# Optimization experiments

Hardware: AMD Instinct MI355X
Metric: run time of the kernel (lower is better)

Reference implementation:

```python
import jax, jax.numpy as jnp
import numpy as np

DIM, DEPTH, MULT = 512, 3, 4
E = 2 ** DEPTH            # 8 experts
HID = MULT * DIM          # 2048
B, S = 4, 1024


def setup_inputs() -> dict:
    key = jax.random.key(0)
    ks = jax.random.split(key, 7)
    sd = 1.0 / np.sqrt(DIM)
    sh = 1.0 / np.sqrt(HID)
    return {
        "x": jax.random.normal(ks[0], (B, S, DIM), dtype=jnp.float32),
        "rw": jax.random.normal(ks[1], (E - 1, DIM), dtype=jnp.float32) * sd,
        "rb": jax.random.normal(ks[2], (E - 1,), dtype=jnp.float32) * sd,
        "w1": jax.random.normal(ks[3], (E, DIM, HID), dtype=jnp.float32) * sd,
        "b1": jax.random.normal(ks[4], (E, HID), dtype=jnp.float32) * sd,
        "w2": jax.random.normal(ks[5], (E, HID, DIM), dtype=jnp.float32) * sh,
        "b2": jax.random.normal(ks[6], (E, DIM), dtype=jnp.float32) * sh,
    }


def _leaf_probs(flat_x, rw, rb):
    # Binary-tree soft routing: level d has 2**d routers at offset 2**d - 1.
    n_tok = flat_x.shape[0]
    leaf = jnp.ones((n_tok, 1), dtype=flat_x.dtype)
    for d in range(DEPTH):
        off, n = 2 ** d - 1, 2 ** d
        logits = flat_x @ rw[off:off + n].T + rb[off:off + n]   # [N, n]
        p = jax.nn.sigmoid(logits)
        # child probs: left = 1-p, right = p
        leaf = (leaf[:, :, None] * jnp.stack([1.0 - p, p], axis=2)).reshape(n_tok, 2 * n)
    return leaf  # [N, E]


def reference(x, rw, rb, w1, b1, w2, b2):
    b, s, dim = x.shape
    flat_x = x.reshape(b * s, dim)                               # [N, D]
    leaf_probs = _leaf_probs(flat_x, rw, rb)                     # [N, E]
    # Dense evaluation of all experts (soft-routing training path).
    h = jnp.einsum('nd,edh->neh', flat_x, w1) + b1[None]         # [N, E, H]
    h = jax.nn.gelu(h, approximate=False)                        # torch nn.GELU (erf)
    y = jnp.einsum('neh,ehd->ned', h, w2) + b2[None]             # [N, E, D]
    out = jnp.einsum('ned,ne->nd', y, leaf_probs)                # [N, D]
    return out.reshape(b, s, dim)
```

## Files before the change

### kernel.cpp

```cpp
#include <hip/hip_runtime.h>
#include <hip/hip_bf16.h>
#include <hip/hip_fp16.h>

#define DIM 512
#define HID 2048
#define NE 8
#define NTOK 4096

typedef _Float16 v8h __attribute__((ext_vector_type(8)));
typedef float v4f __attribute__((ext_vector_type(4)));

__device__ __forceinline__ void load16(const void* g, void* l) {
  __builtin_amdgcn_global_load_lds(
      (const __attribute__((address_space(1))) unsigned int*)g,
      (__attribute__((address_space(3))) unsigned int*)l, 16, 0, 0);
}

__device__ __forceinline__ float gelu_fast(float v) {
  float v2 = v * v;
  float u = v * __builtin_fmaf(0.07135481627f, v2, 1.5957691216f);
  float t = __expf(-u);
  return v * __builtin_amdgcn_rcpf(1.0f + t);
}

__global__ __launch_bounds__(256) void routing_kernel(const float* __restrict__ x,
                                                      const float* __restrict__ rw,
                                                      const float* __restrict__ rb,
                                                      const float* __restrict__ b2,
                                                      float* __restrict__ leaf,
                                                      _Float16* __restrict__ xh,
                                                      float* __restrict__ out) {
  const int lane = threadIdx.x & 63;
  const int wave = threadIdx.x >> 6;
  const int n = (blockIdx.x << 2) + wave;
  const float4* xv = (const float4*)(x + (size_t)n * DIM);
  const float4 x0 = xv[lane * 2], x1 = xv[lane * 2 + 1];
  v8h o;
  o[0] = (_Float16)x0.x; o[1] = (_Float16)x0.y; o[2] = (_Float16)x0.z; o[3] = (_Float16)x0.w;
  o[4] = (_Float16)x1.x; o[5] = (_Float16)x1.y; o[6] = (_Float16)x1.z; o[7] = (_Float16)x1.w;
  *(v8h*)(xh + (size_t)n * DIM + lane * 8) = o;
  float logits[7];
#pragma unroll
  for (int rr = 0; rr < 7; ++rr) {
    const float4* wv = (const float4*)(rw + rr * DIM);
    const float4 w0 = wv[lane * 2], w1v = wv[lane * 2 + 1];
    float s = x0.x * w0.x + x0.y * w0.y + x0.z * w0.z + x0.w * w0.w +
              x1.x * w1v.x + x1.y * w1v.y + x1.z * w1v.z + x1.w * w1v.w;
#pragma unroll
    for (int o2 = 32; o2; o2 >>= 1) s += __shfl_xor(s, o2, 64);
    logits[rr] = s + rb[rr];
  }
  const int eidx = lane & 7;
  const float p0 = 1.f / (1.f + __expf(-logits[0]));
  float f = ((eidx >> 2) & 1) ? p0 : 1.f - p0;
  const float p1 = 1.f / (1.f + __expf(-logits[1 + (eidx >> 2)]));
  f *= ((eidx >> 1) & 1) ? p1 : 1.f - p1;
  const float p2 = 1.f / (1.f + __expf(-logits[3 + (eidx >> 1)]));
  f *= (eidx & 1) ? p2 : 1.f - p2;
  if (lane < NE) leaf[(size_t)n * NE + lane] = f;
  float le[NE];
#pragma unroll
  for (int e = 0; e < NE; ++e) le[e] = __shfl(f, e, 64);
  float4 a0 = {0.f, 0.f, 0.f, 0.f}, a1 = {0.f, 0.f, 0.f, 0.f};
#pragma unroll
  for (int e = 0; e < NE; ++e) {
    const float4* bv = (const float4*)(b2 + (size_t)e * DIM + lane * 8);
    const float4 u0 = bv[0], u1 = bv[1];
    a0.x += le[e] * u0.x; a0.y += le[e] * u0.y; a0.z += le[e] * u0.z; a0.w += le[e] * u0.w;
    a1.x += le[e] * u1.x; a1.y += le[e] * u1.y; a1.z += le[e] * u1.z; a1.w += le[e] * u1.w;
  }
  float4* op = (float4*)(out + (size_t)n * DIM + lane * 8);
  op[0] = a0; op[1] = a1;
}

__global__ __launch_bounds__(256) void transpose_cvt2_kernel(const float* __restrict__ w1,
                                                             _Float16* __restrict__ w1t,
                                                             const float* __restrict__ w2,
                                                             _Float16* __restrict__ w2t) {
  int bx = blockIdx.x;
  const float* in;
  _Float16* outp;
  int R, C;
  if (bx < 4096) { in = w1; outp = w1t; R = DIM; C = HID; }
  else { bx -= 4096; in = w2; outp = w2t; R = HID; C = DIM; }
  const int e = bx >> 9;
  const int rem = bx & 511;
  const int tiles_r = R >> 6;
  const int rt = rem % tiles_r;
  const int ct = rem / tiles_r;
  const int r0 = rt << 6, c0 = ct << 5;
  const size_t ebase = (size_t)e * R * C;

  __shared__ float tile[32][65];
  const int tid = threadIdx.x;
#pragma unroll
  for (int it = 0; it < 2; ++it) {
    const int s = tid + (it << 8);
    const int row = s >> 3, cq = s & 7;
    const float4 v = *(const float4*)(in + ebase + (size_t)(r0 + row) * C + c0 + (cq << 2));
    tile[(cq << 2) + 0][row] = v.x;
    tile[(cq << 2) + 1][row] = v.y;
    tile[(cq << 2) + 2][row] = v.z;
    tile[(cq << 2) + 3][row] = v.w;
  }
  __syncthreads();
  const int c = tid >> 3, seg = tid & 7;
  v8h h;
#pragma unroll
  for (int u = 0; u < 8; ++u) h[u] = (_Float16)tile[c][(seg << 3) + u];
  *(v8h*)(outp + ebase + (size_t)(c0 + c) * R + r0 + (seg << 3)) = h;
}

__global__ __launch_bounds__(256) void gemm1_kernel(const _Float16* __restrict__ xh,
                                                    const _Float16* __restrict__ w1t,
                                                    const float* __restrict__ b1,
                                                    const float* __restrict__ leaf,
                                                    _Float16* __restrict__ H) {
  const int bx = blockIdx.x;
  const int e = bx & 7;
  const int t = bx >> 3;
  const int mt = t & 31;
  const int nt = t >> 5;
  const int m0 = mt << 7, n0 = nt << 7;

  __shared__ alignas(16) _Float16 As[2 * 8192];
  __shared__ alignas(16) _Float16 Bs[2 * 8192];

  const int tid = threadIdx.x;
  const int lane = tid & 63;
  const int wave = tid >> 6;
  const int qm = wave >> 1, qn = wave & 1;
  const int r = lane & 15, q = lane >> 4;

  const _Float16* pa[4];
  const _Float16* pb[4];
  _Float16* la[4];
  _Float16* lb[4];
#pragma unroll
  for (int i = 0; i < 4; ++i) {
    const int ch = (wave << 8) + (i << 6) + lane;
    const int row = ch >> 3;
    const int c8 = (ch & 7) ^ (row & 7);
    pa[i] = xh + (size_t)(m0 + row) * DIM + (c8 << 3);
    pb[i] = w1t + ((size_t)e * HID + n0 + row) * DIM + (c8 << 3);
    la[i] = As + (size_t)ch * 8;
    lb[i] = Bs + (size_t)ch * 8;
  }
  const _Float16* fa[2][4];
  const _Float16* fb[2][4];
#pragma unroll
  for (int ks = 0; ks < 2; ++ks) {
#pragma unroll
    for (int i = 0; i < 4; ++i) {
      const int rowa = (qm << 6) + (i << 4) + r;
      fa[ks][i] = As + (rowa << 6) + ((((ks << 2) + q) ^ (rowa & 7)) << 3);
      const int rowb = (qn << 6) + (i << 4) + r;
      fb[ks][i] = Bs + (rowb << 6) + ((((ks << 2) + q) ^ (rowb & 7)) << 3);
    }
  }

  v4f acc[4][4];
#pragma unroll
  for (int i = 0; i < 4; ++i)
#pragma unroll
    for (int j = 0; j < 4; ++j) acc[i][j] = v4f{0.f, 0.f, 0.f, 0.f};

#pragma unroll
  for (int i = 0; i < 4; ++i) { load16(pa[i], la[i]); load16(pb[i], lb[i]); }

#pragma unroll
  for (int kk = 0; kk < 8; ++kk) {
    __syncthreads();
    if (kk < 7) {
      const int off = (((kk + 1) & 1) << 13);
#pragma unroll
      for (int i = 0; i < 4; ++i) {
        load16(pa[i] + (kk + 1) * 64, la[i] + off);
        load16(pb[i] + (kk + 1) * 64, lb[i] + off);
      }
    }
    const int cp = ((kk & 1) << 13);
#pragma unroll
    for (int ks = 0; ks < 2; ++ks) {
      v8h a[4], b[4];
#pragma unroll
      for (int i = 0; i < 4; ++i) a[i] = *(const v8h*)(fa[ks][i] + cp);
#pragma unroll
      for (int j = 0; j < 4; ++j) b[j] = *(const v8h*)(fb[ks][j] + cp);
#pragma unroll
      for (int i = 0; i < 4; ++i)
#pragma unroll
        for (int j = 0; j < 4; ++j)
          acc[i][j] = __builtin_amdgcn_mfma_f32_16x16x32_f16(a[i], b[j], acc[i][j], 0, 0, 0);
    }
  }

  const float* b1e = b1 + (size_t)e * HID;
  _Float16* He = H + (size_t)e * NTOK * HID;
  float bias[4];
#pragma unroll
  for (int j = 0; j < 4; ++j) bias[j] = b1e[n0 + (qn << 6) + (j << 4) + r];
#pragma unroll
  for (int i = 0; i < 4; ++i) {
    const int rowb = m0 + (qm << 6) + (i << 4) + (q << 2);
#pragma unroll
    for (int rr = 0; rr < 4; ++rr) {
      const int row = rowb + rr;
      const float p = leaf[(size_t)row * NE + e];
      _Float16* hp = He + (size_t)row * HID + n0 + (qn << 6) + r;
#pragma unroll
      for (int j = 0; j < 4; ++j)
        hp[j << 4] = (_Float16)(p * gelu_fast(acc[i][j][rr] + bias[j]));
    }
  }
}

__global__ __launch_bounds__(256) void gemm2_kernel(const _Float16* __restrict__ H,
                                                    const _Float16* __restrict__ w2t,
                                                    float* __restrict__ out) {
  const int bx = blockIdx.x;
  const int e = bx & 7;
  const int mt = (bx >> 3) & 31;
  const int dt = bx >> 8;
  const int m0 = mt << 7, d0 = dt << 7;

  __shared__ alignas(16) _Float16 As[2 * 8192];
  __shared__ alignas(16) _Float16 Bs[2 * 8192];

  const int tid = threadIdx.x;
  const int lane = tid & 63;
  const int wave = tid >> 6;
  const int qm = wave >> 1, qn = wave & 1;
  const int r = lane & 15, q = lane >> 4;

  const _Float16* pa[4];
  const _Float16* pb[4];
  _Float16* la[4];
  _Float16* lb[4];
#pragma unroll
  for (int i = 0; i < 4; ++i) {
    const int ch = (wave << 8) + (i << 6) + lane;
    const int row = ch >> 3;
    const int c8 = (ch & 7) ^ (row & 7);
    pa[i] = H + ((size_t)e * NTOK + m0 + row) * HID + (c8 << 3);
    pb[i] = w2t + ((size_t)e * DIM + d0 + row) * HID + (c8 << 3);
    la[i] = As + (size_t)ch * 8;
    lb[i] = Bs + (size_t)ch * 8;
  }
  const _Float16* fa[2][4];
  const _Float16* fb[2][4];
#pragma unroll
  for (int ks = 0; ks < 2; ++ks) {
#pragma unroll
    for (int i = 0; i < 4; ++i) {
      const int rowa = (qm << 6) + (i << 4) + r;
      fa[ks][i] = As + (rowa << 6) + ((((ks << 2) + q) ^ (rowa & 7)) << 3);
      const int rowb = (qn << 6) + (i << 4) + r;
      fb[ks][i] = Bs + (rowb << 6) + ((((ks << 2) + q) ^ (rowb & 7)) << 3);
    }
  }

  v4f acc[4][4];
#pragma unroll
  for (int i = 0; i < 4; ++i)
#pragma unroll
    for (int j = 0; j < 4; ++j) acc[i][j] = v4f{0.f, 0.f, 0.f, 0.f};

#pragma unroll
  for (int i = 0; i < 4; ++i) { load16(pa[i], la[i]); load16(pb[i], lb[i]); }

  for (int ko = 0; ko < 4; ++ko) {
#pragma unroll
    for (int u = 0; u < 8; ++u) {
      __syncthreads();
      if (!(ko == 3 && u == 7)) {
        const int off = (((u + 1) & 1) << 13);
#pragma unroll
        for (int i = 0; i < 4; ++i) {
          load16(pa[i] + (u + 1) * 64, la[i] + off);
          load16(pb[i] + (u + 1) * 64, lb[i] + off);
        }
      }
      const int cp = ((u & 1) << 13);
#pragma unroll
      for (int ks = 0; ks < 2; ++ks) {
        v8h a[4], b[4];
#pragma unroll
        for (int i = 0; i < 4; ++i) a[i] = *(const v8h*)(fa[ks][i] + cp);
#pragma unroll
        for (int j = 0; j < 4; ++j) b[j] = *(const v8h*)(fb[ks][j] + cp);
#pragma unroll
        for (int i = 0; i < 4; ++i)
#pragma unroll
          for (int j = 0; j < 4; ++j)
            acc[i][j] = __builtin_amdgcn_mfma_f32_16x16x32_f16(a[i], b[j], acc[i][j], 0, 0, 0);
      }
    }
#pragma unroll
    for (int i = 0; i < 4; ++i) { pa[i] += 512; pb[i] += 512; }
  }

#pragma unroll
  for (int i = 0; i < 4; ++i) {
    const int rowb = m0 + (qm << 6) + (i << 4) + (q << 2);
#pragma unroll
    for (int j = 0; j < 4; ++j) {
      const int col = d0 + (qn << 6) + (j << 4) + r;
#pragma unroll
      for (int rr = 0; rr < 4; ++rr)
        atomicAdd(out + (size_t)(rowb + rr) * DIM + col, acc[i][j][rr]);
    }
  }
}

extern "C" void kernel_launch(void* const* d_in, const int* in_sizes, int n_in,
                              void* d_out, int out_size, void* d_ws, size_t ws_size,
                              hipStream_t stream) {
  const float* x  = (const float*)d_in[0];
  const float* rw = (const float*)d_in[1];
  const float* rb = (const float*)d_in[2];
  const float* w1 = (const float*)d_in[3];
  const float* b1 = (const float*)d_in[4];
  const float* w2 = (const float*)d_in[5];
  const float* b2 = (const float*)d_in[6];
  float* out = (float*)d_out;

  char* ws = (char*)d_ws;
  const size_t xh_bytes   = (size_t)NTOK * DIM * 2;
  const size_t w1t_bytes  = (size_t)NE * HID * DIM * 2;
  const size_t w2t_bytes  = (size_t)NE * DIM * HID * 2;
  const size_t leaf_bytes = (size_t)NTOK * NE * 4;
  const size_t H_bytes    = (size_t)NE * NTOK * HID * 2;
  _Float16* xh   = (_Float16*)(ws);
  _Float16* w1t  = (_Float16*)(ws + xh_bytes);
  _Float16* w2t  = (_Float16*)(ws + xh_bytes + w1t_bytes);
  float*    leaf = (float*)(ws + xh_bytes + w1t_bytes + w2t_bytes);
  _Float16* Hbuf = (_Float16*)(ws + xh_bytes + w1t_bytes + w2t_bytes + leaf_bytes);
  if (ws_size < xh_bytes + w1t_bytes + w2t_bytes + leaf_bytes + H_bytes) return;

  routing_kernel<<<1024, 256, 0, stream>>>(x, rw, rb, b2, leaf, xh, out);
  transpose_cvt2_kernel<<<8192, 256, 0, stream>>>(w1, w1t, w2, w2t);
  gemm1_kernel<<<4096, 256, 0, stream>>>(xh, w1t, b1, leaf, Hbuf);
  gemm2_kernel<<<1024, 256, 0, stream>>>(Hbuf, w2t, out);
}
```

Before: 359.5 us.

## Use 256x128 tiles with 32x32 MFMA and merge preprocessing kernels

Both expert GEMMs move from 128x128 tiles on 16x16x32 MFMA to 256x128 tiles on 32x32x16 MFMA, with each wave computing 128x64. This gives more reuse per LDS load and halves the block count. The double-buffered prefetch is replaced by a single buffer with load, sync, compute, sync, so global-to-LDS transfers no longer overlap with math. Routing and the weight transpose/convert are merged into one launch to save launch overhead.

```diff
diff --git a/kernel.cpp b/kernel.cpp
--- a/kernel.cpp
+++ b/kernel.cpp
@@ -8,7 +8,7 @@
 #define NTOK 4096
 
 typedef _Float16 v8h __attribute__((ext_vector_type(8)));
-typedef float v4f __attribute__((ext_vector_type(4)));
+typedef float v16f __attribute__((ext_vector_type(16)));
 
 __device__ __forceinline__ void load16(const void* g, void* l) {
   __builtin_amdgcn_global_load_lds(
@@ -23,292 +23,285 @@
   return v * __builtin_amdgcn_rcpf(1.0f + t);
 }
 
-__global__ __launch_bounds__(256) void routing_kernel(const float* __restrict__ x,
-                                                      const float* __restrict__ rw,
-                                                      const float* __restrict__ rb,
-                                                      const float* __restrict__ b2,
-                                                      float* __restrict__ leaf,
-                                                      _Float16* __restrict__ xh,
-                                                      float* __restrict__ out) {
-  const int lane = threadIdx.x & 63;
-  const int wave = threadIdx.x >> 6;
-  const int n = (blockIdx.x << 2) + wave;
-  const float4* xv = (const float4*)(x + (size_t)n * DIM);
-  const float4 x0 = xv[lane * 2], x1 = xv[lane * 2 + 1];
-  v8h o;
-  o[0] = (_Float16)x0.x; o[1] = (_Float16)x0.y; o[2] = (_Float16)x0.z; o[3] = (_Float16)x0.w;
-  o[4] = (_Float16)x1.x; o[5] = (_Float16)x1.y; o[6] = (_Float16)x1.z; o[7] = (_Float16)x1.w;
-  *(v8h*)(xh + (size_t)n * DIM + lane * 8) = o;
-  float logits[7];
-#pragma unroll
-  for (int rr = 0; rr < 7; ++rr) {
-    const float4* wv = (const float4*)(rw + rr * DIM);
-    const float4 w0 = wv[lane * 2], w1v = wv[lane * 2 + 1];
-    float s = x0.x * w0.x + x0.y * w0.y + x0.z * w0.z + x0.w * w0.w +
-              x1.x * w1v.x + x1.y * w1v.y + x1.z * w1v.z + x1.w * w1v.w;
-#pragma unroll
-    for (int o2 = 32; o2; o2 >>= 1) s += __shfl_xor(s, o2, 64);
-    logits[rr] = s + rb[rr];
-  }
-  const int eidx = lane & 7;
-  const float p0 = 1.f / (1.f + __expf(-logits[0]));
-  float f = ((eidx >> 2) & 1) ? p0 : 1.f - p0;
-  const float p1 = 1.f / (1.f + __expf(-logits[1 + (eidx >> 2)]));
-  f *= ((eidx >> 1) & 1) ? p1 : 1.f - p1;
-  const float p2 = 1.f / (1.f + __expf(-logits[3 + (eidx >> 1)]));
-  f *= (eidx & 1) ? p2 : 1.f - p2;
-  if (lane < NE) leaf[(size_t)n * NE + lane] = f;
-  float le[NE];
-#pragma unroll
-  for (int e = 0; e < NE; ++e) le[e] = __shfl(f, e, 64);
-  float4 a0 = {0.f, 0.f, 0.f, 0.f}, a1 = {0.f, 0.f, 0.f, 0.f};
-#pragma unroll
-  for (int e = 0; e < NE; ++e) {
-    const float4* bv = (const float4*)(b2 + (size_t)e * DIM + lane * 8);
-    const float4 u0 = bv[0], u1 = bv[1];
-    a0.x += le[e] * u0.x; a0.y += le[e] * u0.y; a0.z += le[e] * u0.z; a0.w += le[e] * u0.w;
-    a1.x += le[e] * u1.x; a1.y += le[e] * u1.y; a1.z += le[e] * u1.z; a1.w += le[e] * u1.w;
-  }
-  float4* op = (float4*)(out + (size_t)n * DIM + lane * 8);
-  op[0] = a0; op[1] = a1;
-}
-
-__global__ __launch_bounds__(256) void transpose_cvt2_kernel(const float* __restrict__ w1,
-                                                             _Float16* __restrict__ w1t,
-                                                             const float* __restrict__ w2,
-                                                             _Float16* __restrict__ w2t) {
-  int bx = blockIdx.x;
-  const float* in;
-  _Float16* outp;
-  int R, C;
-  if (bx < 4096) { in = w1; outp = w1t; R = DIM; C = HID; }
-  else { bx -= 4096; in = w2; outp = w2t; R = HID; C = DIM; }
-  const int e = bx >> 9;
-  const int rem = bx & 511;
-  const int tiles_r = R >> 6;
-  const int rt = rem % tiles_r;
-  const int ct = rem / tiles_r;
-  const int r0 = rt << 6, c0 = ct << 5;
-  const size_t ebase = (size_t)e * R * C;
-
+__global__ __launch_bounds__(256) void pre_kernel(const float* __restrict__ x,
+                                                  const float* __restrict__ rw,
+                                                  const float* __restrict__ rb,
+                                                  const float* __restrict__ b2,
+                                                  const float* __restrict__ w1,
+                                                  const float* __restrict__ w2,
+                                                  float* __restrict__ leaf,
+                                                  _Float16* __restrict__ xh,
+                                                  float* __restrict__ out,
+                                                  _Float16* __restrict__ w1t,
+                                                  _Float16* __restrict__ w2t) {
   __shared__ float tile[32][65];
-  const int tid = threadIdx.x;
-#pragma unroll
-  for (int it = 0; it < 2; ++it) {
-    const int s = tid + (it << 8);
-    const int row = s >> 3, cq = s & 7;
-    const float4 v = *(const float4*)(in + ebase + (size_t)(r0 + row) * C + c0 + (cq << 2));
-    tile[(cq << 2) + 0][row] = v.x;
-    tile[(cq << 2) + 1][row] = v.y;
-    tile[(cq << 2) + 2][row] = v.z;
-    tile[(cq << 2) + 3][row] = v.w;
-  }
-  __syncthreads();
-  const int c = tid >> 3, seg = tid & 7;
-  v8h h;
-#pragma unroll
-  for (int u = 0; u < 8; ++u) h[u] = (_Float16)tile[c][(seg << 3) + u];
-  *(v8h*)(outp + ebase + (size_t)(c0 + c) * R + r0 + (seg << 3)) = h;
-}
-
-__global__ __launch_bounds__(256) void gemm1_kernel(const _Float16* __restrict__ xh,
-                                                    const _Float16* __restrict__ w1t,
-                                                    const float* __restrict__ b1,
-                                                    const float* __restrict__ leaf,
-                                                    _Float16* __restrict__ H) {
+  if (blockIdx.x < 1024) {
+    const int lane = threadIdx.x & 63;
+    const int wave = threadIdx.x >> 6;
+    const int n = (blockIdx.x << 2) + wave;
+    const float4* xv = (const float4*)(x + (size_t)n * DIM);
+    const float4 x0 = xv[lane * 2], x1 = xv[lane * 2 + 1];
+    v8h o;
+    o[0] = (_Float16)x0.x; o[1] = (_Float16)x0.y; o[2] = (_Float16)x0.z; o[3] = (_Float16)x0.w;
+    o[4] = (_Float16)x1.x; o[5] = (_Float16)x1.y; o[6] = (_Float16)x1.z; o[7] = (_Float16)x1.w;
+    *(v8h*)(xh + (size_t)n * DIM + lane * 8) = o;
+    float logits[7];
+#pragma unroll
+    for (int rr = 0; rr < 7; ++rr) {
+      const float4* wv = (const float4*)(rw + rr * DIM);
+      const float4 w0 = wv[lane * 2], w1v = wv[lane * 2 + 1];
+      float s = x0.x * w0.x + x0.y * w0.y + x0.z * w0.z + x0.w * w0.w +
+                x1.x * w1v.x + x1.y * w1v.y + x1.z * w1v.z + x1.w * w1v.w;
+#pragma unroll
+      for (int o2 = 32; o2; o2 >>= 1) s += __shfl_xor(s, o2, 64);
+      logits[rr] = s + rb[rr];
+    }
+    const int eidx = lane & 7;
+    const float p0 = 1.f / (1.f + __expf(-logits[0]));
+    float f = ((eidx >> 2) & 1) ? p0 : 1.f - p0;
+    const float p1 = 1.f / (1.f + __expf(-logits[1 + (eidx >> 2)]));
+    f *= ((eidx >> 1) & 1) ? p1 : 1.f - p1;
+    const float p2 = 1.f / (1.f + __expf(-logits[3 + (eidx >> 1)]));
+    f *= (eidx & 1) ? p2 : 1.f - p2;
+    if (lane < NE) leaf[(size_t)n * NE + lane] = f;
+    float le[NE];
+#pragma unroll
+    for (int e = 0; e < NE; ++e) le[e] = __shfl(f, e, 64);
+    float4 a0 = {0.f, 0.f, 0.f, 0.f}, a1 = {0.f, 0.f, 0.f, 0.f};
+#pragma unroll
+    for (int e = 0; e < NE; ++e) {
+      const float4* bv = (const float4*)(b2 + (size_t)e * DIM + lane * 8);
+      const float4 u0 = bv[0], u1 = bv[1];
+      a0.x += le[e] * u0.x; a0.y += le[e] * u0.y; a0.z += le[e] * u0.z; a0.w += le[e] * u0.w;
+      a1.x += le[e] * u1.x; a1.y += le[e] * u1.y; a1.z += le[e] * u1.z; a1.w += le[e] * u1.w;
+    }
+    float4* op = (float4*)(out + (size_t)n * DIM + lane * 8);
+    op[0] = a0; op[1] = a1;
+  } else {
+    int bx = blockIdx.x - 1024;
+    const float* in;
+    _Float16* outp;
+    int R, C;
+    if (bx < 4096) { in = w1; outp = w1t; R = DIM; C = HID; }
+    else { bx -= 4096; in = w2; outp = w2t; R = HID; C = DIM; }
+    const int e = bx >> 9;
+    const int rem = bx & 511;
+    const int tiles_r = R >> 6;
+    const int rt = rem % tiles_r;
+    const int ct = rem / tiles_r;
+    const int r0 = rt << 6, c0 = ct << 5;
+    const size_t ebase = (size_t)e * R * C;
+    const int tid = threadIdx.x;
+#pragma unroll
+    for (int it = 0; it < 2; ++it) {
+      const int s = tid + (it << 8);
+      const int row = s >> 3, cq = s & 7;
+      const float4 v = *(const float4*)(in + ebase + (size_t)(r0 + row) * C + c0 + (cq << 2));
+      tile[(cq << 2) + 0][row] = v.x;
+      tile[(cq << 2) + 1][row] = v.y;
+      tile[(cq << 2) + 2][row] = v.z;
+      tile[(cq << 2) + 3][row] = v.w;
+    }
+    __syncthreads();
+    const int c = tid >> 3, seg = tid & 7;
+    v8h hv;
+#pragma unroll
+    for (int u = 0; u < 8; ++u) hv[u] = (_Float16)tile[c][(seg << 3) + u];
+    *(v8h*)(outp + ebase + (size_t)(c0 + c) * R + r0 + (seg << 3)) = hv;
+  }
+}
+
+__global__ __launch_bounds__(256, 2) void gemm1_kernel(const _Float16* __restrict__ xh,
+                                                       const _Float16* __restrict__ w1t,
+                                                       const float* __restrict__ b1,
+                                                       const float* __restrict__ leaf,
+                                                       _Float16* __restrict__ H) {
   const int bx = blockIdx.x;
   const int e = bx & 7;
   const int t = bx >> 3;
-  const int mt = t & 31;
-  const int nt = t >> 5;
-  const int m0 = mt << 7, n0 = nt << 7;
-
-  __shared__ alignas(16) _Float16 As[2 * 8192];
-  __shared__ alignas(16) _Float16 Bs[2 * 8192];
+  const int mt = t & 15;
+  const int nt = t >> 4;
+  const int m0 = mt << 8, n0 = nt << 7;
+
+  __shared__ alignas(16) _Float16 As[256 * 64];
+  __shared__ alignas(16) _Float16 Bs[128 * 64];
 
   const int tid = threadIdx.x;
   const int lane = tid & 63;
   const int wave = tid >> 6;
-  const int qm = wave >> 1, qn = wave & 1;
-  const int r = lane & 15, q = lane >> 4;
-
-  const _Float16* pa[4];
+  const int wm = wave >> 1, wn = wave & 1;
+  const int c = lane & 31, h2 = lane >> 5;
+  const int cx = c & 7;
+
+  const int strow = tid >> 3;
+  const int c8 = (tid & 7) ^ (strow & 7);
+  const _Float16* pa[8];
   const _Float16* pb[4];
-  _Float16* la[4];
+  _Float16* la[8];
   _Float16* lb[4];
 #pragma unroll
+  for (int i = 0; i < 8; ++i) {
+    pa[i] = xh + (size_t)(m0 + strow + 32 * i) * DIM + (c8 << 3);
+    la[i] = As + tid * 8 + i * 2048;
+  }
+#pragma unroll
   for (int i = 0; i < 4; ++i) {
-    const int ch = (wave << 8) + (i << 6) + lane;
-    const int row = ch >> 3;
-    const int c8 = (ch & 7) ^ (row & 7);
-    pa[i] = xh + (size_t)(m0 + row) * DIM + (c8 << 3);
-    pb[i] = w1t + ((size_t)e * HID + n0 + row) * DIM + (c8 << 3);
-    la[i] = As + (size_t)ch * 8;
-    lb[i] = Bs + (size_t)ch * 8;
-  }
-  const _Float16* fa[2][4];
-  const _Float16* fb[2][4];
-#pragma unroll
-  for (int ks = 0; ks < 2; ++ks) {
-#pragma unroll
-    for (int i = 0; i < 4; ++i) {
-      const int rowa = (qm << 6) + (i << 4) + r;
-      fa[ks][i] = As + (rowa << 6) + ((((ks << 2) + q) ^ (rowa & 7)) << 3);
-      const int rowb = (qn << 6) + (i << 4) + r;
-      fb[ks][i] = Bs + (rowb << 6) + ((((ks << 2) + q) ^ (rowb & 7)) << 3);
-    }
-  }
-
-  v4f acc[4][4];
+    pb[i] = w1t + ((size_t)e * HID + n0 + strow + 32 * i) * DIM + (c8 << 3);
+    lb[i] = Bs + tid * 8 + i * 2048;
+  }
+  const _Float16* fA[4];
+  const _Float16* fB[2];
+#pragma unroll
+  for (int i = 0; i < 4; ++i) fA[i] = As + ((wm << 7) + (i << 5) + c) * 64;
+#pragma unroll
+  for (int j = 0; j < 2; ++j) fB[j] = Bs + ((wn << 6) + (j << 5) + c) * 64;
+
+  v16f acc[4][2];
 #pragma unroll
   for (int i = 0; i < 4; ++i)
 #pragma unroll
-    for (int j = 0; j < 4; ++j) acc[i][j] = v4f{0.f, 0.f, 0.f, 0.f};
-
-#pragma unroll
-  for (int i = 0; i < 4; ++i) { load16(pa[i], la[i]); load16(pb[i], lb[i]); }
+    for (int j = 0; j < 2; ++j)
+      acc[i][j] = v16f{0.f,0.f,0.f,0.f,0.f,0.f,0.f,0.f,0.f,0.f,0.f,0.f,0.f,0.f,0.f,0.f};
 
 #pragma unroll
   for (int kk = 0; kk < 8; ++kk) {
+#pragma unroll
+    for (int i = 0; i < 8; ++i) load16(pa[i] + kk * 64, la[i]);
+#pragma unroll
+    for (int i = 0; i < 4; ++i) load16(pb[i] + kk * 64, lb[i]);
     __syncthreads();
-    if (kk < 7) {
-      const int off = (((kk + 1) & 1) << 13);
-#pragma unroll
-      for (int i = 0; i < 4; ++i) {
-        load16(pa[i] + (kk + 1) * 64, la[i] + off);
-        load16(pb[i] + (kk + 1) * 64, lb[i] + off);
-      }
-    }
-    const int cp = ((kk & 1) << 13);
-#pragma unroll
-    for (int ks = 0; ks < 2; ++ks) {
-      v8h a[4], b[4];
-#pragma unroll
-      for (int i = 0; i < 4; ++i) a[i] = *(const v8h*)(fa[ks][i] + cp);
-#pragma unroll
-      for (int j = 0; j < 4; ++j) b[j] = *(const v8h*)(fb[ks][j] + cp);
+#pragma unroll
+    for (int ks = 0; ks < 4; ++ks) {
+      const int so = ((((ks << 1) + h2) ^ cx) << 3);
+      v8h a[4], b[2];
+#pragma unroll
+      for (int i = 0; i < 4; ++i) a[i] = *(const v8h*)(fA[i] + so);
+#pragma unroll
+      for (int j = 0; j < 2; ++j) b[j] = *(const v8h*)(fB[j] + so);
 #pragma unroll
       for (int i = 0; i < 4; ++i)
 #pragma unroll
-        for (int j = 0; j < 4; ++j)
-          acc[i][j] = __builtin_amdgcn_mfma_f32_16x16x32_f16(a[i], b[j], acc[i][j], 0, 0, 0);
-    }
+        for (int j = 0; j < 2; ++j)
+          acc[i][j] = __builtin_amdgcn_mfma_f32_32x32x16_f16(a[i], b[j], acc[i][j], 0, 0, 0);
+    }
+    __syncthreads();
   }
 
   const float* b1e = b1 + (size_t)e * HID;
   _Float16* He = H + (size_t)e * NTOK * HID;
-  float bias[4];
-#pragma unroll
-  for (int j = 0; j < 4; ++j) bias[j] = b1e[n0 + (qn << 6) + (j << 4) + r];
+  const int colb = n0 + (wn << 6) + c;
+  const float bias0 = b1e[colb];
+  const float bias1 = b1e[colb + 32];
 #pragma unroll
   for (int i = 0; i < 4; ++i) {
-    const int rowb = m0 + (qm << 6) + (i << 4) + (q << 2);
-#pragma unroll
-    for (int rr = 0; rr < 4; ++rr) {
-      const int row = rowb + rr;
-      const float p = leaf[(size_t)row * NE + e];
-      _Float16* hp = He + (size_t)row * HID + n0 + (qn << 6) + r;
-#pragma unroll
-      for (int j = 0; j < 4; ++j)
-        hp[j << 4] = (_Float16)(p * gelu_fast(acc[i][j][rr] + bias[j]));
-    }
-  }
-}
-
-__global__ __launch_bounds__(256) void gemm2_kernel(const _Float16* __restrict__ H,
-                                                    const _Float16* __restrict__ w2t,
-                                                    float* __restrict__ out) {
+    const int rb0 = m0 + (wm << 7) + (i << 5) + (h2 << 2);
+#pragma unroll
+    for (int rg = 0; rg < 4; ++rg) {
+#pragma unroll
+      for (int rr = 0; rr < 4; ++rr) {
+        const int row = rb0 + (rg << 3) + rr;
+        const int reg = (rg << 2) + rr;
+        const float p = leaf[(size_t)row * NE + e];
+        _Float16* hp = He + (size_t)row * HID + colb;
+        hp[0]  = (_Float16)(p * gelu_fast(acc[i][0][reg] + bias0));
+        hp[32] = (_Float16)(p * gelu_fast(acc[i][1][reg] + bias1));
+      }
+    }
+  }
+}
+
+__global__ __launch_bounds__(256, 2) void gemm2_kernel(const _Float16* __restrict__ H,
+                                                       const _Float16* __restrict__ w2t,
+                                                       float* __restrict__ out) {
   const int bx = blockIdx.x;
   const int e = bx & 7;
-  const int mt = (bx >> 3) & 31;
-  const int dt = bx >> 8;
-  const int m0 = mt << 7, d0 = dt << 7;
-
-  __shared__ alignas(16) _Float16 As[2 * 8192];
-  __shared__ alignas(16) _Float16 Bs[2 * 8192];
+  const int dt = (bx >> 3) & 3;
+  const int mt = bx >> 5;
+  const int m0 = mt << 8, d0 = dt << 7;
+
+  __shared__ alignas(16) _Float16 As[256 * 64];
+  __shared__ alignas(16) _Float16 Bs[128 * 64];
 
   const int tid = threadIdx.x;
   const int lane = tid & 63;
   const int wave = tid >> 6;
-  const int qm = wave >> 1, qn = wave & 1;
-  const int r = lane & 15, q = lane >> 4;
-
-  const _Float16* pa[4];
+  const int wm = wave >> 1, wn = wave & 1;
+  const int c = lane & 31, h2 = lane >> 5;
+  const int cx = c & 7;
+
+  const int strow = tid >> 3;
+  const int c8 = (tid & 7) ^ (strow & 7);
+  const _Float16* pa[8];
   const _Float16* pb[4];
-  _Float16* la[4];
+  _Float16* la[8];
   _Float16* lb[4];
 #pragma unroll
+  for (int i = 0; i < 8; ++i) {
+    pa[i] = H + ((size_t)e * NTOK + m0 + strow + 32 * i) * HID + (c8 << 3);
+    la[i] = As + tid * 8 + i * 2048;
+  }
+#pragma unroll
   for (int i = 0; i < 4; ++i) {
-    const int ch = (wave << 8) + (i << 6) + lane;
-    const int row = ch >> 3;
-    const int c8 = (ch & 7) ^ (row & 7);
-    pa[i] = H + ((size_t)e * NTOK + m0 + row) * HID + (c8 << 3);
-    pb[i] = w2t + ((size_t)e * DIM + d0 + row) * HID + (c8 << 3);
-    la[i] = As + (size_t)ch * 8;
-    lb[i] = Bs + (size_t)ch * 8;
-  }
-  const _Float16* fa[2][4];
-  const _Float16* fb[2][4];
-#pragma unroll
-  for (int ks = 0; ks < 2; ++ks) {
-#pragma unroll
-    for (int i = 0; i < 4; ++i) {
-      const int rowa = (qm << 6) + (i << 4) + r;
-      fa[ks][i] = As + (rowa << 6) + ((((ks << 2) + q) ^ (rowa & 7)) << 3);
-      const int rowb = (qn << 6) + (i << 4) + r;
-      fb[ks][i] = Bs + (rowb << 6) + ((((ks << 2) + q) ^ (rowb & 7)) << 3);
-    }
-  }
-
-  v4f acc[4][4];
+    pb[i] = w2t + ((size_t)e * DIM + d0 + strow + 32 * i) * HID + (c8 << 3);
+    lb[i] = Bs + tid * 8 + i * 2048;
+  }
+  const _Float16* fA[4];
+  const _Float16* fB[2];
+#pragma unroll
+  for (int i = 0; i < 4; ++i) fA[i] = As + ((wm << 7) + (i << 5) + c) * 64;
+#pragma unroll
+  for (int j = 0; j < 2; ++j) fB[j] = Bs + ((wn << 6) + (j << 5) + c) * 64;
+
+  v16f acc[4][2];
 #pragma unroll
   for (int i = 0; i < 4; ++i)
 #pragma unroll
-    for (int j = 0; j < 4; ++j) acc[i][j] = v4f{0.f, 0.f, 0.f, 0.f};
-
-#pragma unroll
-  for (int i = 0; i < 4; ++i) { load16(pa[i], la[i]); load16(pb[i], lb[i]); }
+    for (int j = 0; j < 2; ++j)
+      acc[i][j] = v16f{0.f,0.f,0.f,0.f,0.f,0.f,0.f,0.f,0.f,0.f,0.f,0.f,0.f,0.f,0.f,0.f};
 
   for (int ko = 0; ko < 4; ++ko) {
 #pragma unroll
     for (int u = 0; u < 8; ++u) {
+#pragma unroll
+      for (int i = 0; i < 8; ++i) load16(pa[i] + u * 64, la[i]);
+#pragma unroll
+      for (int i = 0; i < 4; ++i) load16(pb[i] + u * 64, lb[i]);
       __syncthreads();
-      if (!(ko == 3 && u == 7)) {
-        const int off = (((u + 1) & 1) << 13);
-#pragma unroll
-        for (int i = 0; i < 4; ++i) {
-          load16(pa[i] + (u + 1) * 64, la[i] + off);
-          load16(pb[i] + (u + 1) * 64, lb[i] + off);
-        }
+#pragma unroll
+      for (int ks = 0; ks < 4; ++ks) {
+        const int so = ((((ks << 1) + h2) ^ cx) << 3);
+        v8h a[4], b[2];
+#pragma unroll
+        for (int i = 0; i < 4; ++i) a[i] = *(const v8h*)(fA[i] + so);
+#pragma unroll
+        for (int j = 0; j < 2; ++j) b[j] = *(const v8h*)(fB[j] + so);
+#pragma unroll
+        for (int i = 0; i < 4; ++i)
+#pragma unroll
+          for (int j = 0; j < 2; ++j)
+            acc[i][j] = __builtin_amdgcn_mfma_f32_32x32x16_f16(a[i], b[j], acc[i][j], 0, 0, 0);
       }
-      const int cp = ((u & 1) << 13);
-#pragma unroll
-      for (int ks = 0; ks < 2; ++ks) {
-        v8h a[4], b[4];
-#pragma unroll
-        for (int i = 0; i < 4; ++i) a[i] = *(const v8h*)(fa[ks][i] + cp);
-#pragma unroll
-        for (int j = 0; j < 4; ++j) b[j] = *(const v8h*)(fb[ks][j] + cp);
-#pragma unroll
-        for (int i = 0; i < 4; ++i)
-#pragma unroll
-          for (int j = 0; j < 4; ++j)
-            acc[i][j] = __builtin_amdgcn_mfma_f32_16x16x32_f16(a[i], b[j], acc[i][j], 0, 0, 0);
+      __syncthreads();
+    }
+#pragma unroll
+    for (int i = 0; i < 8; ++i) pa[i] += 512;
+#pragma unroll
+    for (int i = 0; i < 4; ++i) pb[i] += 512;
+  }
+
+#pragma unroll
+  for (int i = 0; i < 4; ++i) {
+    const int rb0 = m0 + (wm << 7) + (i << 5) + (h2 << 2);
+#pragma unroll
+    for (int rg = 0; rg < 4; ++rg) {
+#pragma unroll
+      for (int rr = 0; rr < 4; ++rr) {
+        const int row = rb0 + (rg << 3) + rr;
+        const int reg = (rg << 2) + rr;
+        float* op = out + (size_t)row * DIM + d0 + (wn << 6) + c;
+        atomicAdd(op, acc[i][0][reg]);
+        atomicAdd(op + 32, acc[i][1][reg]);
       }
-    }
-#pragma unroll
-    for (int i = 0; i < 4; ++i) { pa[i] += 512; pb[i] += 512; }
-  }
-
-#pragma unroll
-  for (int i = 0; i < 4; ++i) {
-    const int rowb = m0 + (qm << 6) + (i << 4) + (q << 2);
-#pragma unroll
-    for (int j = 0; j < 4; ++j) {
-      const int col = d0 + (qn << 6) + (j << 4) + r;
-#pragma unroll
-      for (int rr = 0; rr < 4; ++rr)
-        atomicAdd(out + (size_t)(rowb + rr) * DIM + col, acc[i][j][rr]);
     }
   }
 }
@@ -338,8 +331,7 @@
   _Float16* Hbuf = (_Float16*)(ws + xh_bytes + w1t_bytes + w2t_bytes + leaf_bytes);
   if (ws_size < xh_bytes + w1t_bytes + w2t_bytes + leaf_bytes + H_bytes) return;
 
-  routing_kernel<<<1024, 256, 0, stream>>>(x, rw, rb, b2, leaf, xh, out);
-  transpose_cvt2_kernel<<<8192, 256, 0, stream>>>(w1, w1t, w2, w2t);
-  gemm1_kernel<<<4096, 256, 0, stream>>>(xh, w1t, b1, leaf, Hbuf);
-  gemm2_kernel<<<1024, 256, 0, stream>>>(Hbuf, w2t, out);
-}
+  pre_kernel<<<9216, 256, 0, stream>>>(x, rw, rb, b2, w1, w2, leaf, xh, out, w1t, w2t);
+  gemm1_kernel<<<2048, 256, 0, stream>>>(xh, w1t, b1, leaf, Hbuf);
+  gemm2_kernel<<<512, 256, 0, stream>>>(Hbuf, w2t, out);
+}
```

New measurement: 328.4 us. -8.7%, faster.
